# Performance work log

Measured on AMD Instinct MI355X. Metric: run time of the kernel, lower is better.

## Reference

```python
import jax, jax.numpy as jnp
import numpy as np

N_NODES = 100000
N_EDGES = 1600000
IN_DIM, HID_DIM, LAT_DIM = 128, 64, 32


def _glorot(key, fan_in, fan_out):
    lim = np.sqrt(6.0 / (fan_in + fan_out)).astype(np.float32)
    return jax.random.uniform(key, (fan_in, fan_out), jnp.float32, -lim, lim)


def gcn_layer(x, src, dst, dinv, W, b, n_nodes):
    # PyG GCNConv: out = D^{-1/2} (A + I) D^{-1/2} X W + b
    h = x @ W                                   # [N, F_out]
    norm = dinv[src] * dinv[dst]                # [E+N]
    msg = h[src] * norm[:, None]                # gather + scale
    out = jax.ops.segment_sum(msg, dst, num_segments=n_nodes)  # scatter-add
    return out + b


def _prep_edges(edge_index, n_nodes, dtype):
    loops = jnp.arange(n_nodes, dtype=edge_index.dtype)
    src = jnp.concatenate([edge_index[0], loops])
    dst = jnp.concatenate([edge_index[1], loops])
    deg = jax.ops.segment_sum(jnp.ones_like(dst, dtype=dtype), dst,
                              num_segments=n_nodes)
    dinv = jnp.where(deg > 0, jax.lax.rsqrt(deg), 0.0)
    return src, dst, dinv


def setup_inputs() -> dict:
    key = jax.random.key(0)
    ks = jax.random.split(key, 8)
    x = jax.random.normal(ks[0], (N_NODES, IN_DIM), jnp.float32)
    edge_index = jax.random.randint(ks[1], (2, N_EDGES), 0, N_NODES,
                                    dtype=jnp.int64)
    W1 = _glorot(ks[2], IN_DIM, HID_DIM)
    b1 = jnp.zeros((HID_DIM,), jnp.float32)
    W2 = _glorot(ks[3], HID_DIM, HID_DIM)
    b2 = jnp.zeros((HID_DIM,), jnp.float32)
    W3 = _glorot(ks[4], HID_DIM, LAT_DIM)
    b3 = jnp.zeros((LAT_DIM,), jnp.float32)
    return {"x": x, "edge_index": edge_index,
            "W1": W1, "b1": b1, "W2": W2, "b2": b2, "W3": W3, "b3": b3}


def reference(x, edge_index, W1, b1, W2, b2, W3, b3):
    n = x.shape[0]
    src, dst, dinv = _prep_edges(edge_index, n, x.dtype)
    h = jax.nn.relu(gcn_layer(x, src, dst, dinv, W1, b1, n))
    h = jax.nn.relu(gcn_layer(h, src, dst, dinv, W2, b2, n))
    return gcn_layer(h, src, dst, dinv, W3, b3, n)
```

## Files before the change

kernel.cpp:

```cpp
#include <hip/hip_runtime.h>
#include <hip/hip_fp16.h>


#define BSH 7
#define BNODES (1 << BSH)
#define NBUCKET_MAX 1024
#define CAPSH 12
#define BIN_T 1024
#define BIN_E 13

typedef __attribute__((ext_vector_type(4))) _Float16 half4v;
typedef __attribute__((ext_vector_type(4))) float float4v;

__global__ __launch_bounds__(BIN_T) void k_bin(
    const int* __restrict__ src, const int* __restrict__ dst,
    int* __restrict__ bcur, unsigned* __restrict__ ebin, int e, int nb) {
    __shared__ int hist[NBUCKET_MAX];
    const int tid = threadIdx.x;
    for (int b = tid; b < nb; b += BIN_T) hist[b] = 0;
    __syncthreads();

    const int base = blockIdx.x * (BIN_T * BIN_E);
    int      bk[BIN_E];
    unsigned pk[BIN_E];
#pragma unroll
    for (int j = 0; j < BIN_E; ++j) {
        int idx = base + j * BIN_T + tid;
        bk[j] = -1;
        if (idx < e) {
            int d = dst[idx], s = src[idx];
            bk[j] = d >> BSH;
            pk[j] = ((unsigned)s << BSH) | (unsigned)(d & (BNODES - 1));
            atomicAdd(&hist[bk[j]], 1);
        }
    }
    __syncthreads();
    for (int b = tid; b < nb; b += BIN_T) {
        int c = hist[b];
        hist[b] = c ? atomicAdd(&bcur[b], c) : 0;
    }
    __syncthreads();
#pragma unroll
    for (int j = 0; j < BIN_E; ++j) {
        if (bk[j] >= 0) {
            int pos = atomicAdd(&hist[bk[j]], 1);
            ebin[pos] = pk[j];
        }
    }
}

__global__ __launch_bounds__(512) void k_place2(
    const unsigned* __restrict__ ebin, const int* __restrict__ bcur,
    int* __restrict__ esrc, int* __restrict__ cnt, int* __restrict__ offs,
    float* __restrict__ dinv, int n) {
    __shared__ int hist[BNODES];
    __shared__ int loff[BNODES];
    __shared__ int cur[BNODES];
    const int b = blockIdx.x, tid = threadIdx.x;
    const int node0 = b << BSH;
    const int start = b << CAPSH;
    const int end   = bcur[b];
    if (tid < BNODES) hist[tid] = 0;
    __syncthreads();
    for (int j = start + tid; j < end; j += 512)
        atomicAdd(&hist[ebin[j] & (BNODES - 1)], 1);
    __syncthreads();
    int v  = (tid < BNODES) ? hist[tid] : 0;
    int vp = (v + 7) & ~7;
    if (tid < BNODES) loff[tid] = vp;
    __syncthreads();
    for (int off = 1; off < BNODES; off <<= 1) {
        int add = (tid < BNODES && tid >= off) ? loff[tid - off] : 0;
        __syncthreads();
        if (tid < BNODES) loff[tid] += add;
        __syncthreads();
    }
    if (tid < BNODES) {
        int o = start + loff[tid] - vp;
        cur[tid] = o;
        int node = node0 + tid;
        if (node < n) {
            cnt[node]  = vp;
            offs[node] = o;
            dinv[node] = rsqrtf((float)(v + 1));
        }
    }
    __syncthreads();
    const int total = loff[BNODES - 1];
    for (int i = start + tid; i < start + total; i += 512)
        esrc[i] = n;
    __syncthreads();
    for (int j = start + tid; j < end; j += 512) {
        unsigned p = ebin[j];
        int pos = atomicAdd(&cur[p & (BNODES - 1)], 1);
        esrc[pos] = (int)(p >> BSH);
    }
}

__global__ __launch_bounds__(256) void k_wprep(
    const float* __restrict__ W1, const float* __restrict__ W2,
    const float* __restrict__ W3, __half* __restrict__ wt1,
    __half* __restrict__ wt2, __half* __restrict__ wt3,
    __half* __restrict__ g, __half* __restrict__ g3,
    int* __restrict__ bcur, int n, int nb) {
    int gid = blockIdx.x * 256 + threadIdx.x;
    if (gid < 8192) {
        int k = gid >> 6, f = gid & 63;
        wt1[f * 136 + k] = __float2half(W1[gid]);
    } else if (gid < 12288) {
        int i = gid - 8192;
        int k = i >> 6, f = i & 63;
        wt2[f * 72 + k] = __float2half(W2[i]);
    } else if (gid < 14336) {
        int i = gid - 12288;
        int k = i >> 5, f = i & 31;
        wt3[f * 72 + k] = __float2half(W3[i]);
    } else if (gid < 14400) {
        g[(size_t)n * 64 + (gid - 14336)] = __float2half(0.f);
    } else if (gid < 14432) {
        g3[(size_t)n * 32 + (gid - 14400)] = __float2half(0.f);
    } else if (gid < 14432 + nb) {
        int b = gid - 14432;
        bcur[b] = b << CAPSH;
    }
}

template <int K, int F, typename InT>
__global__ __launch_bounds__(256) void k_gemm_mfma(
    const InT* __restrict__ in, const __half* __restrict__ wt_img,
    const float* __restrict__ dinv, __half* __restrict__ g, int n) {
    constexpr int KP = K + 8;
    constexpr int FP = F + 8;
    constexpr int NT = 64;
    constexpr int CT = F / 16;
    __shared__ __align__(16) __half xs[NT][KP];
    __shared__ __align__(16) __half wt[F][KP];
    const int tid = threadIdx.x;
    const int node0 = blockIdx.x * NT;

    if constexpr (sizeof(InT) == 4) {
        constexpr int KW = K / 4;
        const float4* in4 = reinterpret_cast<const float4*>(in);
        for (int i = tid; i < NT * KW; i += 256) {
            int r = i / KW, c = (i % KW) * 4;
            if (node0 + r < n) {
                float4 v = in4[(size_t)(node0 + r) * KW + (i % KW)];
                union { __half2 h2[2]; uint2 u; } pk;
                pk.h2[0] = __floats2half2_rn(v.x, v.y);
                pk.h2[1] = __floats2half2_rn(v.z, v.w);
                *reinterpret_cast<uint2*>(&xs[r][c]) = pk.u;
            }
        }
    } else {
        constexpr int KW = K / 8;
        const uint4* in4 = reinterpret_cast<const uint4*>(in);
        for (int i = tid; i < NT * KW; i += 256) {
            int r = i / KW, c = (i % KW) * 8;
            if (node0 + r < n)
                *reinterpret_cast<uint4*>(&xs[r][c]) =
                    in4[(size_t)(node0 + r) * KW + (i % KW)];
        }
    }
    {
        const uint4* wim = reinterpret_cast<const uint4*>(wt_img);
        uint4* wt4 = reinterpret_cast<uint4*>(&wt[0][0]);
        for (int i = tid; i < F * KP / 8; i += 256) wt4[i] = wim[i];
    }
    __syncthreads();

    const int wid = tid >> 6, lane = tid & 63;
    const int rl = lane & 15;
    const int kb = (lane >> 4) * 4;
    const int arow = wid * 16 + rl;

    float4v acc[CT];
#pragma unroll
    for (int c = 0; c < CT; ++c) acc[c] = (float4v)(0.f);

#pragma unroll
    for (int kk = 0; kk < K / 16; ++kk) {
        union { uint2 u; half4v h; } a;
        a.u = *reinterpret_cast<const uint2*>(&xs[arow][kk * 16 + kb]);
#pragma unroll
        for (int c = 0; c < CT; ++c) {
            union { uint2 u; half4v h; } b;
            b.u = *reinterpret_cast<const uint2*>(&wt[c * 16 + rl][kk * 16 + kb]);
            acc[c] = __builtin_amdgcn_mfma_f32_16x16x16f16(a.h, b.h, acc[c], 0, 0, 0);
        }
    }
    __syncthreads();

    __half (*hs)[FP] = reinterpret_cast<__half (*)[FP]>(&xs[0][0]);
    float dv[4];
#pragma unroll
    for (int i = 0; i < 4; ++i) {
        int r = wid * 16 + (lane >> 4) * 4 + i;
        dv[i] = (node0 + r < n) ? dinv[node0 + r] : 0.f;
    }
#pragma unroll
    for (int c = 0; c < CT; ++c)
#pragma unroll
        for (int i = 0; i < 4; ++i) {
            int r = wid * 16 + (lane >> 4) * 4 + i;
            hs[r][c * 16 + rl] = __float2half(acc[c][i] * dv[i]);
        }
    __syncthreads();
    constexpr int FW = F / 8;
    for (int i = tid; i < NT * FW; i += 256) {
        int r = i / FW, c = (i % FW) * 8;
        if (node0 + r < n)
            *reinterpret_cast<uint4*>(&g[(size_t)(node0 + r) * F + c]) =
                *reinterpret_cast<const uint4*>(&hs[r][c]);
    }
}

__device__ inline void h8_acc(uint4 u, float* a) {
    const __half2* h = reinterpret_cast<const __half2*>(&u);
#pragma unroll
    for (int i = 0; i < 4; ++i) {
        float2 f = __half22float2(h[i]);
        a[2 * i]     += f.x;
        a[2 * i + 1] += f.y;
    }
}

__device__ inline void h8_acc2(uint4 ua, uint4 ub, float* a) {
    const __half2* ha = reinterpret_cast<const __half2*>(&ua);
    const __half2* hb = reinterpret_cast<const __half2*>(&ub);
#pragma unroll
    for (int i = 0; i < 4; ++i) {
        __half2 s = __hadd2(ha[i], hb[i]);
        float2 f = __half22float2(s);
        a[2 * i]     += f.x;
        a[2 * i + 1] += f.y;
    }
}

template <int F, bool RELU, bool HOUT>
__global__ __launch_bounds__(256, 6) void k_agg(
    const __half* __restrict__ gin, const int* __restrict__ offs,
    const int* __restrict__ cnt, const int* __restrict__ esrc,
    const float* __restrict__ dinv, const float* __restrict__ bias,
    __half* __restrict__ hout, float* __restrict__ fout, int n) {
    constexpr int LPN = F / 8;
    constexpr int NPW = 64 / LPN;
    constexpr int RS  = F / 8;
    const int wid  = threadIdx.x >> 6;
    const int lane = threadIdx.x & 63;
    const int sub  = lane / LPN;
    const int fl   = lane % LPN;
    const int node = (blockIdx.x * 4 + wid) * NPW + sub;
    if (node >= n) return;
    const int start = offs[node];
    const int m     = cnt[node];
    const uint4* gp = reinterpret_cast<const uint4*>(gin) + fl;

    float acc[8];
#pragma unroll
    for (int i = 0; i < 8; ++i) acc[i] = 0.f;

    int4 ia = {0, 0, 0, 0}, ib = {0, 0, 0, 0};
    if (m > 0) {
        ia = *reinterpret_cast<const int4*>(esrc + start);
        ib = *reinterpret_cast<const int4*>(esrc + start + 4);
    }
    for (int j = 0; j < m; j += 8) {
        uint4 r0 = gp[(size_t)ia.x * RS];
        uint4 r1 = gp[(size_t)ia.y * RS];
        uint4 r2 = gp[(size_t)ia.z * RS];
        uint4 r3 = gp[(size_t)ia.w * RS];
        uint4 r4 = gp[(size_t)ib.x * RS];
        uint4 r5 = gp[(size_t)ib.y * RS];
        uint4 r6 = gp[(size_t)ib.z * RS];
        uint4 r7 = gp[(size_t)ib.w * RS];
        if (j + 8 < m) {
            ia = *reinterpret_cast<const int4*>(esrc + start + j + 8);
            ib = *reinterpret_cast<const int4*>(esrc + start + j + 12);
        }
        h8_acc2(r0, r1, acc);
        h8_acc2(r2, r3, acc);
        h8_acc2(r4, r5, acc);
        h8_acc2(r6, r7, acc);
    }

    float sv[8];
#pragma unroll
    for (int i = 0; i < 8; ++i) sv[i] = 0.f;
    h8_acc(gp[(size_t)node * RS], sv);
    const float dv = dinv[node];
    float4 b0 = *reinterpret_cast<const float4*>(bias + fl * 8);
    float4 b1 = *reinterpret_cast<const float4*>(bias + fl * 8 + 4);
    float bb[8] = {b0.x, b0.y, b0.z, b0.w, b1.x, b1.y, b1.z, b1.w};
    float rr[8];
#pragma unroll
    for (int i = 0; i < 8; ++i) {
        rr[i] = dv * (acc[i] + sv[i]) + bb[i];
        if (RELU) rr[i] = fmaxf(rr[i], 0.f);
    }
    if (HOUT) {
        union { __half2 h2[4]; uint4 u; } pk;
#pragma unroll
        for (int i = 0; i < 4; ++i)
            pk.h2[i] = __floats2half2_rn(rr[2 * i], rr[2 * i + 1]);
        reinterpret_cast<uint4*>(hout)[(size_t)node * RS + fl] = pk.u;
    } else {
        float4 o0 = {rr[0], rr[1], rr[2], rr[3]};
        float4 o1 = {rr[4], rr[5], rr[6], rr[7]};
        float4* fo = reinterpret_cast<float4*>(fout) + (size_t)node * (F / 4) + fl * 2;
        fo[0] = o0;
        fo[1] = o1;
    }
}

extern "C" void kernel_launch(void* const* d_in, const int* in_sizes, int n_in,
                              void* d_out, int out_size, void* d_ws, size_t ws_size,
                              hipStream_t stream) {
    const float* x  = (const float*)d_in[0];
    const int*   ei = (const int*)d_in[1];
    const float* W1 = (const float*)d_in[2];
    const float* b1 = (const float*)d_in[3];
    const float* W2 = (const float*)d_in[4];
    const float* b2 = (const float*)d_in[5];
    const float* W3 = (const float*)d_in[6];
    const float* b3 = (const float*)d_in[7];
    float* out = (float*)d_out;

    const int n = in_sizes[0] / 128;
    const int e = in_sizes[1] / 2;
    const int* src = ei;
    const int* dst = ei + e;

    const int nb = (n + BNODES - 1) >> BSH;

    float*    dinv = (float*)d_ws;
    __half*   g    = (__half*)(dinv + n);
    __half*   h16  = (__half*)((int*)d_ws + n + (size_t)n * 32 + 32);
    __half*   g3   = h16 + (size_t)n * 64;
    int*      cnt  = (int*)(g3 + (size_t)n * 32 + 32);
    int*      offs = cnt + n;
    int*      bcur = offs + n;
    __half*   wt1  = (__half*)(bcur + NBUCKET_MAX);
    __half*   wt2  = wt1 + 64 * 136;
    __half*   wt3  = wt2 + 64 * 72;
    unsigned* ebin = (unsigned*)(wt3 + 32 * 72 + 32);
    int*      esrc = (int*)(ebin + ((size_t)nb << CAPSH));

    const int B = 256;
    const int binGrid = (e + BIN_T * BIN_E - 1) / (BIN_T * BIN_E);

    k_wprep<<<60, B, 0, stream>>>(W1, W2, W3, wt1, wt2, wt3, g, g3, bcur, n, nb);
    k_bin<<<binGrid, BIN_T, 0, stream>>>(src, dst, bcur, ebin, e, nb);
    k_place2<<<nb, 512, 0, stream>>>(ebin, bcur, esrc, cnt, offs, dinv, n);

    k_gemm_mfma<128, 64, float><<<(n + 63) / 64, B, 0, stream>>>(x, wt1, dinv, g, n);
    k_agg<64, true, true><<<n / 32, B, 0, stream>>>(
        g, offs, cnt, esrc, dinv, b1, h16, nullptr, n);

    k_gemm_mfma<64, 64, __half><<<(n + 63) / 64, B, 0, stream>>>(h16, wt2, dinv, g, n);
    k_agg<64, true, true><<<n / 32, B, 0, stream>>>(
        g, offs, cnt, esrc, dinv, b2, h16, nullptr, n);

    k_gemm_mfma<64, 32, __half><<<(n + 63) / 64, B, 0, stream>>>(h16, wt3, dinv, g3, n);
    k_agg<32, false, false><<<(n + 63) / 64, B, 0, stream>>>(
        g3, offs, cnt, esrc, dinv, b3, nullptr, out, n);
}
```

Before: 154.6 us.

## Sort nodes by padded degree class within each bucket to balance aggregation warps

During CSR placement, each bucket of nodes now gets a counting sort by padded-degree class, producing a node permutation. The aggregation kernels read the node through this permutation, so the nodes sharing a wave have similar edge counts and less lane divergence. This adds one extra indirect load per lane, a small prefix pass in placement, and slightly more launched slots to cover padding. Output locality changes because consecutive lanes now write non-contiguous nodes.

```diff
diff --git a/kernel.cpp b/kernel.cpp
--- a/kernel.cpp
+++ b/kernel.cpp
@@ -52,22 +52,28 @@
 __global__ __launch_bounds__(512) void k_place2(
     const unsigned* __restrict__ ebin, const int* __restrict__ bcur,
     int* __restrict__ esrc, int* __restrict__ cnt, int* __restrict__ offs,
-    float* __restrict__ dinv, int n) {
+    float* __restrict__ dinv, int* __restrict__ nodeperm, int n) {
     __shared__ int hist[BNODES];
     __shared__ int loff[BNODES];
     __shared__ int cur[BNODES];
+    __shared__ int chist[32], ccur[32];
     const int b = blockIdx.x, tid = threadIdx.x;
     const int node0 = b << BSH;
     const int start = b << CAPSH;
     const int end   = bcur[b];
     if (tid < BNODES) hist[tid] = 0;
+    if (tid >= BNODES && tid < BNODES + 32) chist[tid - BNODES] = 0;
     __syncthreads();
     for (int j = start + tid; j < end; j += 512)
         atomicAdd(&hist[ebin[j] & (BNODES - 1)], 1);
     __syncthreads();
     int v  = (tid < BNODES) ? hist[tid] : 0;
     int vp = (v + 7) & ~7;
-    if (tid < BNODES) loff[tid] = vp;
+    int cls = vp >> 3; if (cls > 31) cls = 31;
+    if (tid < BNODES) {
+        loff[tid] = vp;
+        atomicAdd(&chist[cls], 1);
+    }
     __syncthreads();
     for (int off = 1; off < BNODES; off <<= 1) {
         int add = (tid < BNODES && tid >= off) ? loff[tid - off] : 0;
@@ -75,10 +81,18 @@
         if (tid < BNODES) loff[tid] += add;
         __syncthreads();
     }
+    if (tid == 0) {
+        int s = 0;
+#pragma unroll
+        for (int c = 0; c < 32; ++c) { int t = chist[c]; ccur[c] = s; s += t; }
+    }
+    __syncthreads();
     if (tid < BNODES) {
         int o = start + loff[tid] - vp;
         cur[tid] = o;
         int node = node0 + tid;
+        int p = atomicAdd(&ccur[cls], 1);
+        nodeperm[node0 + p] = (node < n) ? node : n;
         if (node < n) {
             cnt[node]  = vp;
             offs[node] = o;
@@ -240,6 +254,7 @@
 __global__ __launch_bounds__(256, 6) void k_agg(
     const __half* __restrict__ gin, const int* __restrict__ offs,
     const int* __restrict__ cnt, const int* __restrict__ esrc,
+    const int* __restrict__ nodeperm,
     const float* __restrict__ dinv, const float* __restrict__ bias,
     __half* __restrict__ hout, float* __restrict__ fout, int n) {
     constexpr int LPN = F / 8;
@@ -249,7 +264,8 @@
     const int lane = threadIdx.x & 63;
     const int sub  = lane / LPN;
     const int fl   = lane % LPN;
-    const int node = (blockIdx.x * 4 + wid) * NPW + sub;
+    const int slot = (blockIdx.x * 4 + wid) * NPW + sub;
+    const int node = nodeperm[slot];
     if (node >= n) return;
     const int start = offs[node];
     const int m     = cnt[node];
@@ -331,6 +347,7 @@
     const int* dst = ei + e;
 
     const int nb = (n + BNODES - 1) >> BSH;
+    const int nslots = nb << BSH;
 
     float*    dinv = (float*)d_ws;
     __half*   g    = (__half*)(dinv + n);
@@ -338,7 +355,8 @@
     __half*   g3   = h16 + (size_t)n * 64;
     int*      cnt  = (int*)(g3 + (size_t)n * 32 + 32);
     int*      offs = cnt + n;
-    int*      bcur = offs + n;
+    int*      perm = offs + n;
+    int*      bcur = perm + nslots;
     __half*   wt1  = (__half*)(bcur + NBUCKET_MAX);
     __half*   wt2  = wt1 + 64 * 136;
     __half*   wt3  = wt2 + 64 * 72;
@@ -350,17 +368,17 @@
 
     k_wprep<<<60, B, 0, stream>>>(W1, W2, W3, wt1, wt2, wt3, g, g3, bcur, n, nb);
     k_bin<<<binGrid, BIN_T, 0, stream>>>(src, dst, bcur, ebin, e, nb);
-    k_place2<<<nb, 512, 0, stream>>>(ebin, bcur, esrc, cnt, offs, dinv, n);
+    k_place2<<<nb, 512, 0, stream>>>(ebin, bcur, esrc, cnt, offs, dinv, perm, n);
 
     k_gemm_mfma<128, 64, float><<<(n + 63) / 64, B, 0, stream>>>(x, wt1, dinv, g, n);
-    k_agg<64, true, true><<<n / 32, B, 0, stream>>>(
-        g, offs, cnt, esrc, dinv, b1, h16, nullptr, n);
+    k_agg<64, true, true><<<nslots / 32, B, 0, stream>>>(
+        g, offs, cnt, esrc, perm, dinv, b1, h16, nullptr, n);
 
     k_gemm_mfma<64, 64, __half><<<(n + 63) / 64, B, 0, stream>>>(h16, wt2, dinv, g, n);
-    k_agg<64, true, true><<<n / 32, B, 0, stream>>>(
-        g, offs, cnt, esrc, dinv, b2, h16, nullptr, n);
+    k_agg<64, true, true><<<nslots / 32, B, 0, stream>>>(
+        g, offs, cnt, esrc, perm, dinv, b2, h16, nullptr, n);
 
     k_gemm_mfma<64, 32, __half><<<(n + 63) / 64, B, 0, stream>>>(h16, wt3, dinv, g3, n);
-    k_agg<32, false, false><<<(n + 63) / 64, B, 0, stream>>>(
-        g3, offs, cnt, esrc, dinv, b3, nullptr, out, n);
-}
+    k_agg<32, false, false><<<nslots / 64, B, 0, stream>>>(
+        g3, offs, cnt, esrc, perm, dinv, b3, nullptr, out, n);
+}
```

Measured after the change: 164.0 us. 1.06x slower.
